# Kernel optimization log

Measured on AMD Instinct MI355X. Metric: run time of the kernel, lower is better.

The kernel has to match this reference:

```python
import jax, jax.numpy as jnp
import numpy as np

S = 8192      # sequence length
D = 768       # bert_out_dim
NA = 256      # num aspects
NO = 256      # num opinions
MAXW = 40     # max span width (width_embedding has 40 entries)
NCAT = 13
NPOL = 3


def setup_inputs() -> dict:
    key = jax.random.key(0)
    ks = jax.random.split(key, 9)
    word_rep = jax.random.normal(ks[0], (S, D), jnp.float32)
    a_head = jax.random.randint(ks[1], (NA,), 0, S - MAXW)
    a_w = jax.random.randint(ks[2], (NA,), 1, MAXW + 1)
    aspects = jnp.stack([a_head, a_head + a_w], axis=-1)  # [NA,2] (head,tail), head<tail
    o_head = jax.random.randint(ks[3], (NO,), 0, S - MAXW)
    o_w = jax.random.randint(ks[4], (NO,), 1, MAXW + 1)
    opinions = jnp.stack([o_head, o_head + o_w], axis=-1)  # [NO,2]
    sc = 0.02
    return {
        'word_rep': word_rep,
        'aspects': aspects,
        'opinions': opinions,
        'W_valid': jax.random.normal(ks[5], (2 * D, 2), jnp.float32) * sc,
        'b_valid': jnp.zeros((2,), jnp.float32),
        'W_cat': jax.random.normal(ks[6], (2 * D, NCAT), jnp.float32) * sc,
        'b_cat': jnp.zeros((NCAT,), jnp.float32),
        'W_pol': jax.random.normal(ks[7], (2 * D, NPOL), jnp.float32) * sc,
        'b_pol': jnp.zeros((NPOL,), jnp.float32),
    }


def _span_maxpool(word_rep, spans):
    # variable-width span max-pool over tokens, vectorized with a gather + mask
    heads, tails = spans[:, 0], spans[:, 1]          # [n]
    pos = heads[:, None] + jnp.arange(MAXW)[None, :]  # [n, MAXW]
    valid = pos < tails[:, None]                      # [n, MAXW]
    g = word_rep[jnp.clip(pos, 0, word_rep.shape[0] - 1)]  # [n, MAXW, D]
    neg = jnp.finfo(word_rep.dtype).min
    return jnp.max(jnp.where(valid[:, :, None], g, neg), axis=1)  # [n, D]


def reference(word_rep, aspects, opinions, W_valid, b_valid, W_cat, b_cat, W_pol, b_pol):
    asp_rep = _span_maxpool(word_rep, aspects)   # [NA, D]
    opi_rep = _span_maxpool(word_rep, opinions)  # [NO, D]
    na, no = asp_rep.shape[0], opi_rep.shape[0]
    # all aspect x opinion pairs (itertools.product order): asp varies slowest
    pair_reps = jnp.concatenate([
        jnp.repeat(asp_rep, no, axis=0),          # [NA*NO, D]
        jnp.tile(opi_rep, (na, 1)),               # [NA*NO, D]
    ], axis=-1)                                    # [NA*NO, 2D]
    asp_ids = jnp.repeat(jnp.arange(na), no)
    opi_ids = jnp.tile(jnp.arange(no), na)

    valid_out = pair_reps @ W_valid + b_valid      # [P, 2]
    cate_out = pair_reps @ W_cat + b_cat           # [P, NCAT]
    polar_out = pair_reps @ W_pol + b_pol          # [P, NPOL]

    valid_mask = valid_out[:, 0] > valid_out[:, 1]  # [P] bool
    # jit-safe masking instead of data-dependent boolean select
    m = valid_mask[:, None]
    return (jnp.where(m, pair_reps, 0.0),
            jnp.where(valid_mask, asp_ids, -1),
            jnp.where(valid_mask, opi_ids, -1),
            jnp.where(m, cate_out, 0.0),
            jnp.where(m, polar_out, 0.0),
            valid_mask)
```

## Files before the change

### kernel.cpp

```cpp
#include <hip/hip_runtime.h>
#include <math.h>

#define S 8192
#define D 768
#define NA 256
#define NO 256
#define MAXW 40
#define NCAT 13
#define NPOL 3
#define NPROJ (2 + NCAT + NPOL)

#define OFF1 ((size_t)NA * NO * 2 * D)
#define OFF2 (OFF1 + (size_t)NA * NO)
#define OFF3 (OFF2 + (size_t)NA * NO)
#define OFF4 (OFF3 + (size_t)NA * NO * NCAT)
#define OFF5 (OFF4 + (size_t)NA * NO * NPOL)

#define NEGF (-3.402823466e+38f)

typedef float vfloat4 __attribute__((ext_vector_type(4)));

__global__ __launch_bounds__(256) void span_pool_proj(
    const float* __restrict__ word_rep,
    const int*   __restrict__ aspects,
    const int*   __restrict__ opinions,
    const float* __restrict__ W_valid,
    const float* __restrict__ W_cat,
    const float* __restrict__ W_pol,
    float*  __restrict__ rep_out,
    double* __restrict__ proj_out)
{
    __shared__ float  rep[D];
    __shared__ double part[4][NPROJ];
    const int b = blockIdx.x;
    const int t = threadIdx.x;

    const int* spans = (b < NA) ? aspects : opinions;
    const int  s     = (b < NA) ? b : (b - NA);
    const int  woff  = (b < NA) ? 0 : D;

    const int head  = spans[2 * s];
    const int tail  = spans[2 * s + 1];
    const int width = tail - head;

    if (t < 192) {
        const vfloat4* base = (const vfloat4*)(word_rep + (size_t)head * D) + t;
        vfloat4 m = base[0];
#pragma unroll
        for (int r = 1; r < MAXW; ++r) {
            vfloat4 v = base[(size_t)r * (D / 4)];
            const bool ok = r < width;
            m.x = fmaxf(m.x, ok ? v.x : NEGF);
            m.y = fmaxf(m.y, ok ? v.y : NEGF);
            m.z = fmaxf(m.z, ok ? v.z : NEGF);
            m.w = fmaxf(m.w, ok ? v.w : NEGF);
        }
        ((vfloat4*)rep)[t] = m;
        ((vfloat4*)(rep_out + (size_t)b * D))[t] = m;
    }
    __syncthreads();

    const int w    = t >> 6;
    const int lane = t & 63;
    if (lane < NPROJ) {
        const float* W; int ncol, col;
        if (lane < 2)           { W = W_valid; ncol = 2;    col = lane; }
        else if (lane < 2+NCAT) { W = W_cat;   ncol = NCAT; col = lane - 2; }
        else                    { W = W_pol;   ncol = NPOL; col = lane - 2 - NCAT; }
        const int d0 = w * (D / 4);
        double a0 = 0.0, a1 = 0.0;
#pragma unroll 8
        for (int d = d0; d < d0 + (D / 4); d += 2) {
            a0 += (double)rep[d]     * (double)W[(size_t)(woff + d)     * ncol + col];
            a1 += (double)rep[d + 1] * (double)W[(size_t)(woff + d + 1) * ncol + col];
        }
        part[w][lane] = a0 + a1;
    }
    __syncthreads();
    if (t < NPROJ)
        proj_out[(size_t)b * NPROJ + t] =
            (part[0][t] + part[1][t]) + (part[2][t] + part[3][t]);
}

#define JPB 64

__global__ __launch_bounds__(384) void pair_out(
    const vfloat4* __restrict__ rep4,
    const double*  __restrict__ proj,
    const float*   __restrict__ b_valid,
    const float*   __restrict__ b_cat,
    const float*   __restrict__ b_pol,
    float*         __restrict__ out)
{
    const int blk = blockIdx.x;
    const int i   = blk >> 2;
    const int j0  = (blk & 3) * JPB;
    const int t   = threadIdx.x;
    const int l   = t & 63;

    const double pa0 = proj[(size_t)i * NPROJ + 0];
    const double pa1 = proj[(size_t)i * NPROJ + 1];
    const double bv0 = (double)b_valid[0];
    const double bv1 = (double)b_valid[1];

    const double q0 = proj[(size_t)(NA + j0 + l) * NPROJ + 0];
    const double q1 = proj[(size_t)(NA + j0 + l) * NPROJ + 1];
    const unsigned long long mb = __ballot((pa0 + q0 + bv0) > (pa1 + q1 + bv1));

    vfloat4 av = (vfloat4)0.f;
    if (t < 192) av = rep4[(size_t)i * 192 + t];

    const int c = t - 192;
    double pac = 0.0; float bias = 0.0f;
    if (c >= 0 && c < 16) {
        pac  = proj[(size_t)i * NPROJ + 2 + c];
        bias = (c < NCAT) ? b_cat[c] : b_pol[c - NCAT];
    }

    const double* po  = proj + (size_t)(NA + j0) * NPROJ;
    vfloat4*      dst = (vfloat4*)out + (size_t)((i << 8) | j0) * 384 + t;

#pragma unroll 4
    for (int jj = 0; jj < JPB; ++jj) {
        const int j = j0 + jj;
        const int p = (i << 8) | j;
        const bool mask = (mb >> jj) & 1ULL;

        vfloat4 src = (t < 192) ? av
                                : rep4[(size_t)(NA + j) * 192 + (t - 192)];
        vfloat4 val = mask ? src : (vfloat4)0.f;
        dst[0] = val;

        if (c >= 0 && c < 16) {
            float v = mask ? (float)(pac + po[2 + c] + (double)bias) : 0.0f;
            if (c < NCAT) out[OFF3 + (size_t)p * NCAT + c] = v;
            else          out[OFF4 + (size_t)p * NPOL + (c - NCAT)] = v;
        } else if (c == 16) {
            out[OFF1 + p] = mask ? (float)i : -1.0f;
        } else if (c == 17) {
            out[OFF2 + p] = mask ? (float)j : -1.0f;
        } else if (c == 18) {
            out[OFF5 + p] = mask ? 1.0f : 0.0f;
        }

        po  += NPROJ;
        dst += 384;
    }
}

extern "C" void kernel_launch(void* const* d_in, const int* in_sizes, int n_in,
                              void* d_out, int out_size, void* d_ws, size_t ws_size,
                              hipStream_t stream)
{
    const float* word_rep = (const float*)d_in[0];
    const int*   aspects  = (const int*)  d_in[1];
    const int*   opinions = (const int*)  d_in[2];
    const float* W_valid  = (const float*)d_in[3];
    const float* b_valid  = (const float*)d_in[4];
    const float* W_cat    = (const float*)d_in[5];
    const float* b_cat    = (const float*)d_in[6];
    const float* W_pol    = (const float*)d_in[7];
    const float* b_pol    = (const float*)d_in[8];
    float* out = (float*)d_out;

    float*  rep  = (float*)d_ws;
    double* proj = (double*)((char*)d_ws + (size_t)(NA + NO) * D * sizeof(float));

    span_pool_proj<<<NA + NO, 256, 0, stream>>>(
        word_rep, aspects, opinions, W_valid, W_cat, W_pol, rep, proj);

    pair_out<<<NA * 4, 384, 0, stream>>>(
        (const vfloat4*)rep, proj, b_valid, b_cat, b_pol, out);
}
```

Baseline: 481.3 us.

## Vectorize small pair outputs and skip span rows beyond width

In pair_out, the scattered per-pair scalar stores for categories, polarities, ids and mask become coalesced float4 stores, each thread filling four contiguous output elements. The rep copy loop is also split by thread half so that only opinion threads load per-j data. In span_pool_proj, rows are read in groups of 8 and the loop exits early once past the span width, avoiding loads of unused rows. The cost is extra integer division/modulo work and some control flow divergence.

```diff
diff --git a/kernel.cpp b/kernel.cpp
--- a/kernel.cpp
+++ b/kernel.cpp
@@ -47,13 +47,18 @@
         const vfloat4* base = (const vfloat4*)(word_rep + (size_t)head * D) + t;
         vfloat4 m = base[0];
 #pragma unroll
-        for (int r = 1; r < MAXW; ++r) {
-            vfloat4 v = base[(size_t)r * (D / 4)];
-            const bool ok = r < width;
-            m.x = fmaxf(m.x, ok ? v.x : NEGF);
-            m.y = fmaxf(m.y, ok ? v.y : NEGF);
-            m.z = fmaxf(m.z, ok ? v.z : NEGF);
-            m.w = fmaxf(m.w, ok ? v.w : NEGF);
+        for (int g = 0; g < MAXW; g += 8) {
+            if (g && g >= width) break;
+            const int rbeg = g ? g : 1;
+#pragma unroll
+            for (int r = rbeg; r < g + 8; ++r) {
+                vfloat4 v = base[(size_t)r * (D / 4)];
+                const bool ok = r < width;
+                m.x = fmaxf(m.x, ok ? v.x : NEGF);
+                m.y = fmaxf(m.y, ok ? v.y : NEGF);
+                m.z = fmaxf(m.z, ok ? v.z : NEGF);
+                m.w = fmaxf(m.w, ok ? v.w : NEGF);
+            }
         }
         ((vfloat4*)rep)[t] = m;
         ((vfloat4*)(rep_out + (size_t)b * D))[t] = m;
@@ -107,44 +112,79 @@
     const double q1 = proj[(size_t)(NA + j0 + l) * NPROJ + 1];
     const unsigned long long mb = __ballot((pa0 + q0 + bv0) > (pa1 + q1 + bv1));
 
-    vfloat4 av = (vfloat4)0.f;
-    if (t < 192) av = rep4[(size_t)i * 192 + t];
-
-    const int c = t - 192;
-    double pac = 0.0; float bias = 0.0f;
-    if (c >= 0 && c < 16) {
-        pac  = proj[(size_t)i * NPROJ + 2 + c];
-        bias = (c < NCAT) ? b_cat[c] : b_pol[c - NCAT];
-    }
-
-    const double* po  = proj + (size_t)(NA + j0) * NPROJ;
-    vfloat4*      dst = (vfloat4*)out + (size_t)((i << 8) | j0) * 384 + t;
-
-#pragma unroll 4
-    for (int jj = 0; jj < JPB; ++jj) {
-        const int j = j0 + jj;
-        const int p = (i << 8) | j;
-        const bool mask = (mb >> jj) & 1ULL;
-
-        vfloat4 src = (t < 192) ? av
-                                : rep4[(size_t)(NA + j) * 192 + (t - 192)];
-        vfloat4 val = mask ? src : (vfloat4)0.f;
-        dst[0] = val;
-
-        if (c >= 0 && c < 16) {
-            float v = mask ? (float)(pac + po[2 + c] + (double)bias) : 0.0f;
-            if (c < NCAT) out[OFF3 + (size_t)p * NCAT + c] = v;
-            else          out[OFF4 + (size_t)p * NPOL + (c - NCAT)] = v;
-        } else if (c == 16) {
-            out[OFF1 + p] = mask ? (float)i : -1.0f;
-        } else if (c == 17) {
-            out[OFF2 + p] = mask ? (float)j : -1.0f;
-        } else if (c == 18) {
-            out[OFF5 + p] = mask ? 1.0f : 0.0f;
-        }
-
-        po  += NPROJ;
-        dst += 384;
+    vfloat4* dst = (vfloat4*)out + (size_t)((i << 8) | j0) * 384 + t;
+
+    if (t < 192) {
+        const vfloat4 av = rep4[(size_t)i * 192 + t];
+#pragma unroll 8
+        for (int jj = 0; jj < JPB; ++jj) {
+            vfloat4 val = ((mb >> jj) & 1ULL) ? av : (vfloat4)0.f;
+            dst[0] = val;
+            dst += 384;
+        }
+    } else {
+        const vfloat4* osrc = rep4 + (size_t)(NA + j0) * 192 + (t - 192);
+#pragma unroll 8
+        for (int jj = 0; jj < JPB; ++jj) {
+            vfloat4 v   = osrc[0];
+            vfloat4 val = ((mb >> jj) & 1ULL) ? v : (vfloat4)0.f;
+            dst[0] = val;
+            osrc += 192;
+            dst  += 384;
+        }
+    }
+
+    const int p0 = (i << 8) | j0;
+
+    if (t < 208) {
+        const int e0 = t * 4;
+        vfloat4 v;
+#pragma unroll
+        for (int k = 0; k < 4; ++k) {
+            const int e  = e0 + k;
+            const int jj = e / NCAT;
+            const int c  = e % NCAT;
+            const bool mk = (mb >> jj) & 1ULL;
+            const double pac = proj[(size_t)i * NPROJ + 2 + c];
+            const double poc = proj[(size_t)(NA + j0 + jj) * NPROJ + 2 + c];
+            v[k] = mk ? (float)(pac + poc + (double)b_cat[c]) : 0.0f;
+        }
+        *(vfloat4*)(out + OFF3 + (size_t)p0 * NCAT + e0) = v;
+    } else if (t < 256) {
+        const int e0 = (t - 208) * 4;
+        vfloat4 v;
+#pragma unroll
+        for (int k = 0; k < 4; ++k) {
+            const int e  = e0 + k;
+            const int jj = e / NPOL;
+            const int c  = e % NPOL;
+            const bool mk = (mb >> jj) & 1ULL;
+            const double pac = proj[(size_t)i * NPROJ + 2 + NCAT + c];
+            const double poc = proj[(size_t)(NA + j0 + jj) * NPROJ + 2 + NCAT + c];
+            v[k] = mk ? (float)(pac + poc + (double)b_pol[c]) : 0.0f;
+        }
+        *(vfloat4*)(out + OFF4 + (size_t)p0 * NPOL + e0) = v;
+    } else if (t < 272) {
+        const int e0 = (t - 256) * 4;
+        vfloat4 v;
+#pragma unroll
+        for (int k = 0; k < 4; ++k)
+            v[k] = ((mb >> (e0 + k)) & 1ULL) ? (float)i : -1.0f;
+        *(vfloat4*)(out + OFF1 + (size_t)p0 + e0) = v;
+    } else if (t < 288) {
+        const int e0 = (t - 272) * 4;
+        vfloat4 v;
+#pragma unroll
+        for (int k = 0; k < 4; ++k)
+            v[k] = ((mb >> (e0 + k)) & 1ULL) ? (float)(j0 + e0 + k) : -1.0f;
+        *(vfloat4*)(out + OFF2 + (size_t)p0 + e0) = v;
+    } else if (t < 304) {
+        const int e0 = (t - 288) * 4;
+        vfloat4 v;
+#pragma unroll
+        for (int k = 0; k < 4; ++k)
+            v[k] = ((mb >> (e0 + k)) & 1ULL) ? 1.0f : 0.0f;
+        *(vfloat4*)(out + OFF5 + (size_t)p0 + e0) = v;
     }
 }
 
```

Result: faster. 446.1 us (-7.3%).
